# Kernel optimization log

Measured on AMD Instinct MI355X. Metric: run time of the kernel, lower is better.

The kernel has to match this reference:

```python
import jax, jax.numpy as jnp
import numpy as np

B, S, D, H = 4, 1024, 1024, 16
HD = D // H


def setup_inputs() -> dict:
    key = jax.random.key(0)
    ks = jax.random.split(key, 12)
    s = 1.0 / np.sqrt(D)
    inp = {
        'q': jax.random.normal(ks[0], (B, S, D), jnp.float32),
        'k': jax.random.normal(ks[1], (B, S, D), jnp.float32),
        'v': jax.random.normal(ks[2], (B, S, D), jnp.float32),
        'mask': jnp.broadcast_to(jnp.tril(jnp.ones((S, S), jnp.int32)), (B, S, S)),
        'Wq': jax.random.uniform(ks[3], (D, D), jnp.float32, -s, s),
        'bq': jax.random.uniform(ks[4], (D,), jnp.float32, -s, s),
        'Wk': jax.random.uniform(ks[5], (D, D), jnp.float32, -s, s),
        'bk': jax.random.uniform(ks[6], (D,), jnp.float32, -s, s),
        'Wv': jax.random.uniform(ks[7], (D, D), jnp.float32, -s, s),
        'bv': jax.random.uniform(ks[8], (D,), jnp.float32, -s, s),
        'Wo': jax.random.uniform(ks[9], (D, D), jnp.float32, -s, s),
        'bo': jax.random.uniform(ks[10], (D,), jnp.float32, -s, s),
    }
    return inp


def _split_heads(x):
    # [B,S,D] -> [B,H,S,HD]
    b, s, d = x.shape
    return x.reshape(b, s, H, HD).transpose(0, 2, 1, 3)


def reference(q, k, v, mask, Wq, bq, Wk, bk, Wv, bv, Wo, bo):
    # Linear projections (torch Linear: x @ W.T + b) followed by relu
    qh = jax.nn.relu(q @ Wq.T + bq)
    kh = jax.nn.relu(k @ Wk.T + bk)
    vh = jax.nn.relu(v @ Wv.T + bv)
    qh, kh, vh = _split_heads(qh), _split_heads(kh), _split_heads(vh)
    scores = jnp.einsum('bhqd,bhkd->bhqk', qh, kh) / jnp.sqrt(jnp.float32(HD))
    scores = jnp.where(mask[:, None, :, :] == 0, jnp.float32(-1e9), scores)
    attn = jax.nn.softmax(scores, axis=-1)
    y = jnp.einsum('bhqk,bhkd->bhqd', attn, vh)
    y = y.transpose(0, 2, 1, 3).reshape(B, S, D)  # merge heads
    return jax.nn.relu(y @ Wo.T + bo)
```

## Files before the change

### kernel.cpp

```cpp
#include <hip/hip_runtime.h>


using f16    = _Float16;
using f16x4  = __attribute__((ext_vector_type(4))) _Float16;
using f16x8  = __attribute__((ext_vector_type(8))) _Float16;
using f32x4  = __attribute__((ext_vector_type(4))) float;
using f32x16 = __attribute__((ext_vector_type(16))) float;

static constexpr int S = 1024, Dm = 1024, NH = 16, HD = 64;

#if __has_builtin(__builtin_amdgcn_mfma_f32_32x32x16_f16)
#define USE_G32 1
#define MFMA32(ACC, A_, B_) \
    (ACC) = __builtin_amdgcn_mfma_f32_32x32x16_f16((A_), (B_), (ACC), 0, 0, 0)
#else
#define USE_G32 0
#endif

#if __has_builtin(__builtin_amdgcn_mfma_f32_16x16x32_f16) && \
    __has_builtin(__builtin_amdgcn_mfma_f32_16x16x16f16)
#define USE_A16 1
#define MFMA16K32(ACC, A_, B_) \
    (ACC) = __builtin_amdgcn_mfma_f32_16x16x32_f16((A_), (B_), (ACC), 0, 0, 0)
#define MFMA16(ACC, A_, B_) \
    (ACC) = __builtin_amdgcn_mfma_f32_16x16x16f16((A_), (B_), (ACC), 0, 0, 0)
#else
#define USE_A16 0
#endif

#define LO4(v) __builtin_shufflevector((v), (v), 0, 1, 2, 3)
#define HI4(v) __builtin_shufflevector((v), (v), 4, 5, 6, 7)

__device__ __forceinline__ f16x4 cvt4(float4 a) {
    f16x4 r; r[0] = (f16)a.x; r[1] = (f16)a.y; r[2] = (f16)a.z; r[3] = (f16)a.w;
    return r;
}

__device__ __forceinline__ int pcol64(int k) {
#if USE_A16
    return ((k >> 3) & 3) * 16 + ((k >> 5) << 3) + (k & 7);
#else
    return ((k >> 2) & 3) * 16 + ((k >> 4) << 2) + (k & 3);
#endif
}

__device__ __forceinline__ int swz(int row, int col) {
    return (col & ~31) | ((((col >> 3) ^ row) & 3) << 3) | (col & 7);
}

__device__ __forceinline__ void store_out(void* out, int mode, int m, int n, float v) {
    if (mode == 2) {
        ((float*)out)[(size_t)m * Dm + n] = v;
    } else {
        const int b_ = m >> 10, s_ = m & 1023, h_ = n >> 6, hd_ = n & 63;
        const size_t idx = (mode == 0)
            ? (((size_t)(b_ * NH + h_) * S + s_) * HD + pcol64(hd_))
            : (((size_t)(b_ * NH + h_) * HD + hd_) * S + s_);
        ((f16*)out)[idx] = (f16)v;
    }
}

#if __has_builtin(__builtin_amdgcn_global_load_lds)
#define HAS_GLL 1
#else
#define HAS_GLL 0
#endif

__device__ __forceinline__ void gll16(const f16* g, f16* l) {
#if HAS_GLL
    __builtin_amdgcn_global_load_lds(
        (const __attribute__((address_space(1))) void*)g,
        (__attribute__((address_space(3))) void*)l, 16, 0, 0);
#else
    *(uint4*)l = *(const uint4*)g;
#endif
}

__global__ __launch_bounds__(256)
void cvt_w(const float* __restrict__ s0, const float* __restrict__ s1,
           const float* __restrict__ s2, f16* __restrict__ dst)
{
    const int z = blockIdx.y;
    const float* src = (z == 0) ? s0 : (z == 1) ? s1 : s2;
    const int e = blockIdx.x * 256 + threadIdx.x;
    const int n = e >> 8;
    const int k = (e & 255) * 4;
    const float4 v = *(const float4*)(src + (size_t)n * Dm + k);
    *(f16x4*)(dst + (size_t)z * Dm * Dm + (size_t)n * Dm + swz(n, k)) = cvt4(v);
}

template <int ADMA>
__device__ __forceinline__ void gemm_core(const void* __restrict__ A,
                                          const f16* __restrict__ Wf,
                                          const float* __restrict__ bias,
                                          void* __restrict__ out, int mode)
{
    const int tid = threadIdx.x;
    const int bm = blockIdx.x, bn = blockIdx.y;
#if USE_G32
    __shared__ alignas(16) f16 As[2][128][ADMA ? 32 : 36];
    __shared__ alignas(16) f16 Ws[2][128][32];

    const int lane = tid & 63, wave = tid >> 6;
    const int l31 = lane & 31, kh = lane >> 5;
    const int wm = wave & 1, wn = wave >> 1;

    const int dr = wave * 16 + (lane >> 2);
    const int dc = (lane & 3) * 8;
    const f16* Wsrc = Wf + (size_t)(bn * 128 + dr) * Dm + dc;
    const f16* Asrc = (const f16*)A + (size_t)(bm * 128 + dr) * Dm + dc;

    const int ar = tid >> 3, ac = (tid & 7) * 4;
    const float* Af = (const float*)A + (size_t)(bm * 128 + ar) * Dm + ac;

    float4 pa[4];
    auto prefA = [&](int k0) {
#pragma unroll
        for (int i = 0; i < 4; ++i) pa[i] = *(const float4*)(Af + k0 + (size_t)i * 32 * Dm);
    };
    auto stageA = [&](int cur) {
#pragma unroll
        for (int i = 0; i < 4; ++i) *(f16x4*)&As[cur][ar + i * 32][ac] = cvt4(pa[i]);
    };
    auto dma = [&](int k0, int cur) {
        gll16(Wsrc + k0, &Ws[cur][dr][dc]);
        gll16(Wsrc + k0 + (size_t)64 * Dm, &Ws[cur][64 + dr][dc]);
        if (ADMA) {
            gll16(Asrc + k0, &As[cur][dr][dc]);
            gll16(Asrc + k0 + (size_t)64 * Dm, &As[cur][64 + dr][dc]);
        }
    };

    f32x16 acc[2][2] = {};
    if (!ADMA) prefA(0);
    dma(0, 0);
    for (int it = 0; it < Dm / 32; ++it) {
        const int cur = it & 1;
        if (!ADMA) stageA(cur);
        __syncthreads();
        if (it < Dm / 32 - 1) {
            if (!ADMA) prefA((it + 1) * 32);
            dma((it + 1) * 32, cur ^ 1);
        }

#pragma unroll
        for (int s2 = 0; s2 < 2; ++s2) {
            const int sl = s2 * 2 + kh;
            f16x8 af[2], bf[2];
#pragma unroll
            for (int g = 0; g < 2; ++g) {
                const int rr = g * 32 + l31;
                const int slot = (sl ^ rr) & 3;
                if (ADMA) {
                    af[g] = *(const f16x8*)&As[cur][wm * 64 + rr][slot * 8];
                } else {
                    const int c = s2 * 16 + kh * 8;
                    const f16x4 lo = *(const f16x4*)&As[cur][wm * 64 + rr][c];
                    const f16x4 hi = *(const f16x4*)&As[cur][wm * 64 + rr][c + 4];
                    af[g] = __builtin_shufflevector(lo, hi, 0, 1, 2, 3, 4, 5, 6, 7);
                }
                bf[g] = *(const f16x8*)&Ws[cur][wn * 64 + rr][slot * 8];
            }
            MFMA32(acc[0][0], af[0], bf[0]);
            MFMA32(acc[0][1], af[0], bf[1]);
            MFMA32(acc[1][0], af[1], bf[0]);
            MFMA32(acc[1][1], af[1], bf[1]);
        }
    }

#pragma unroll
    for (int g2 = 0; g2 < 2; ++g2) {
        const int col = bn * 128 + wn * 64 + g2 * 32 + l31;
        const float bb = bias[col];
#pragma unroll
        for (int g = 0; g < 2; ++g)
#pragma unroll
            for (int blk = 0; blk < 4; ++blk) {
                const int row0 = bm * 128 + wm * 64 + g * 32 + 8 * blk + 4 * kh;
                if (mode == 1) {
                    const int b_ = row0 >> 10, s_ = row0 & 1023;
                    const int h_ = col >> 6, hd_ = col & 63;
                    f16x4 vv;
#pragma unroll
                    for (int r = 0; r < 4; ++r)
                        vv[r] = (f16)fmaxf(acc[g][g2][blk * 4 + r] + bb, 0.0f);
                    *(f16x4*)&((f16*)out)[((size_t)(b_ * NH + h_) * HD + hd_) * S + s_] = vv;
                } else {
#pragma unroll
                    for (int r = 0; r < 4; ++r)
                        store_out(out, mode, row0 + r, col,
                                  fmaxf(acc[g][g2][blk * 4 + r] + bb, 0.0f));
                }
            }
    }
#else
    for (int i = tid; i < 128 * 128; i += 256) {
        const int m = bm * 128 + (i >> 7);
        const int n = bn * 128 + (i & 127);
        float acc = 0.0f;
        for (int k2 = 0; k2 < Dm; ++k2) {
            const float a = ADMA ? (float)((const f16*)A)[(size_t)m * Dm + swz(m, k2)]
                                 : ((const float*)A)[(size_t)m * Dm + k2];
            acc = fmaf(a, (float)Wf[(size_t)n * Dm + swz(n, k2)], acc);
        }
        store_out(out, mode, m, n, fmaxf(acc + bias[n], 0.0f));
    }
#endif
}

__global__ __launch_bounds__(256)
void gemm_qkv(const float* __restrict__ q, const float* __restrict__ k,
              const float* __restrict__ v, const f16* __restrict__ wqkv,
              const float* __restrict__ bq, const float* __restrict__ bk,
              const float* __restrict__ bv,
              f16* __restrict__ qh, f16* __restrict__ kh, f16* __restrict__ vt)
{
    const int z = blockIdx.z;
    const float* A = (z == 0) ? q : (z == 1) ? k : v;
    const float* B = (z == 0) ? bq : (z == 1) ? bk : bv;
    f16* O = (z == 0) ? qh : (z == 1) ? kh : vt;
    gemm_core<0>(A, wqkv + (size_t)z * Dm * Dm, B, O, (z == 2) ? 1 : 0);
}

__global__ __launch_bounds__(256)
void gemm_out(const f16* __restrict__ y, const f16* __restrict__ wo,
              const float* __restrict__ bo, float* __restrict__ out)
{
    gemm_core<1>(y, wo, bo, out, 2);
}

__global__ __launch_bounds__(256)
void attn_fwd(const f16* __restrict__ qh, const f16* __restrict__ kh,
              const f16* __restrict__ vt, f16* __restrict__ y)
{
    const int bz = blockIdx.x;
    const int qt = bz & 15;
    const int h  = (bz >> 4) & 15;
    const int b  = bz >> 8;
    const size_t head = (size_t)(b * NH + h) * S * HD;

#if USE_A16
    __shared__ alignas(16) f16 Ks[2][64][72];
    __shared__ alignas(16) f16 Vs[2][64][72];

    const int tid  = threadIdx.x;
    const int wave = tid >> 6;
    const int lane = tid & 63;
    const int l15  = lane & 15;
    const int quad = lane >> 4;
    const int sr   = tid >> 2;
    const int sc   = (tid & 3) * 16;

    const f16* Qrow = qh + head + (size_t)(qt * 64 + wave * 16 + l15) * HD;
    const f16* Kp   = kh + head;
    const f16* Vp   = vt + head;

    f16x8 aq[2];
    {
        const uint4 q0 = *(const uint4*)(Qrow + quad * 16);
        const uint4 q1 = *(const uint4*)(Qrow + quad * 16 + 8);
        aq[0] = *(f16x8*)&q0;
        aq[1] = *(f16x8*)&q1;
    }

    const int qg = qt * 64 + wave * 16 + l15;
    float m_i = -1e30f, l_i = 0.0f;
    f32x4 acc_o[4] = {};

    uint4 pk[2], pv[2];
    auto pref = [&](int kt) {
        const f16* Kr = Kp + (size_t)(kt * 64 + sr) * HD + sc;
        pk[0] = *(const uint4*)Kr;
        pk[1] = *(const uint4*)(Kr + 8);
        const f16* Vr = Vp + (size_t)sr * S + kt * 64 + sc;
        pv[0] = *(const uint4*)Vr;
        pv[1] = *(const uint4*)(Vr + 8);
    };

    pref(0);
    for (int kt = 0; kt <= qt; ++kt) {
        const int cur = kt & 1;
        *(uint4*)&Ks[cur][sr][sc]     = pk[0];
        *(uint4*)&Ks[cur][sr][sc + 8] = pk[1];
        {
            const int sb = (sc >> 4) * 4;
            *(f16x4*)&Vs[cur][sr][0 * 16 + sb] = *(f16x4*)((f16*)&pv[0]);
            *(f16x4*)&Vs[cur][sr][1 * 16 + sb] = *(f16x4*)((f16*)&pv[0] + 4);
            *(f16x4*)&Vs[cur][sr][2 * 16 + sb] = *(f16x4*)((f16*)&pv[1]);
            *(f16x4*)&Vs[cur][sr][3 * 16 + sb] = *(f16x4*)((f16*)&pv[1] + 4);
        }
        __syncthreads();
        if (kt < qt) pref(kt + 1);

        f32x4 accs[4] = {};
#pragma unroll
        for (int t = 0; t < 4; ++t) {
            const f16x8 k8a = *(const f16x8*)&Ks[cur][t * 16 + l15][quad * 16];
            const f16x8 k8b = *(const f16x8*)&Ks[cur][t * 16 + l15][quad * 16 + 8];
            MFMA16K32(accs[t], k8a, aq[0]);
            MFMA16K32(accs[t], k8b, aq[1]);
        }

        const int key0 = kt * 64 + quad * 4;
#pragma unroll
        for (int t = 0; t < 4; ++t)
#pragma unroll
            for (int r = 0; r < 4; ++r) {
                float sv = accs[t][r] * 0.125f;
                if (key0 + t * 16 + r > qg) sv = -1e9f;
                accs[t][r] = sv;
            }

        float mx = accs[0][0];
#pragma unroll
        for (int t = 0; t < 4; ++t)
#pragma unroll
            for (int r = 0; r < 4; ++r) mx = fmaxf(mx, accs[t][r]);
        mx = fmaxf(mx, __shfl_xor(mx, 16, 64));
        mx = fmaxf(mx, __shfl_xor(mx, 32, 64));
        const float mnew = fmaxf(m_i, mx);
        float sm = 0.0f;
#pragma unroll
        for (int t = 0; t < 4; ++t)
#pragma unroll
            for (int r = 0; r < 4; ++r) {
                const float e = __expf(accs[t][r] - mnew);
                accs[t][r] = e;
                sm += e;
            }
        sm += __shfl_xor(sm, 16, 64);
        sm += __shfl_xor(sm, 32, 64);
        const float alpha = __expf(m_i - mnew);
        l_i = l_i * alpha + sm;
        m_i = mnew;

        f16x4 ap[4];
#pragma unroll
        for (int c = 0; c < 4; ++c) {
            f16x4 v;
#pragma unroll
            for (int j = 0; j < 4; ++j) v[j] = (f16)accs[c][j];
            ap[c] = v;
        }

        float ar[4];
#pragma unroll
        for (int r = 0; r < 4; ++r) ar[r] = __shfl(alpha, quad * 4 + r, 64);
#pragma unroll
        for (int t2 = 0; t2 < 4; ++t2)
#pragma unroll
            for (int r = 0; r < 4; ++r) acc_o[t2][r] *= ar[r];
#pragma unroll
        for (int t2 = 0; t2 < 4; ++t2) {
            const f16x8 v8a = *(const f16x8*)&Vs[cur][t2 * 16 + l15][quad * 16];
            const f16x8 v8b = *(const f16x8*)&Vs[cur][t2 * 16 + l15][quad * 16 + 8];
            MFMA16(acc_o[t2], ap[0], LO4(v8a));
            MFMA16(acc_o[t2], ap[1], HI4(v8a));
            MFMA16(acc_o[t2], ap[2], LO4(v8b));
            MFMA16(acc_o[t2], ap[3], HI4(v8b));
        }
    }

    float lr[4];
#pragma unroll
    for (int r = 0; r < 4; ++r) lr[r] = __shfl(l_i, quad * 4 + r, 64);
#pragma unroll
    for (int t2 = 0; t2 < 4; ++t2)
#pragma unroll
        for (int r = 0; r < 4; ++r) {
            const int srow = qt * 64 + wave * 16 + quad * 4 + r;
            const int dcol = h * 64 + t2 * 16 + l15;
            y[((size_t)b * S + srow) * Dm + swz(srow, dcol)] =
                (f16)(acc_o[t2][r] / lr[r]);
        }
#else
    const int tid = threadIdx.x;
    if (tid < 64) {
        const int q = qt * 64 + tid;
        const f16* Qr = qh + head + (size_t)q * HD;
        float qv[64];
        for (int d = 0; d < 64; ++d) qv[d] = (float)Qr[pcol64(d)];
        float mx = -1e30f;
        for (int key = 0; key <= q; ++key) {
            const f16* Kr = kh + head + (size_t)key * HD;
            float s = 0.0f;
            for (int d = 0; d < 64; ++d) s = fmaf(qv[d], (float)Kr[pcol64(d)], s);
            mx = fmaxf(mx, s * 0.125f);
        }
        float o[64];
        for (int d = 0; d < 64; ++d) o[d] = 0.0f;
        float l = 0.0f;
        for (int key = 0; key <= q; ++key) {
            const f16* Kr = kh + head + (size_t)key * HD;
            float s = 0.0f;
            for (int d = 0; d < 64; ++d) s = fmaf(qv[d], (float)Kr[pcol64(d)], s);
            const float p = __expf(s * 0.125f - mx);
            l += p;
            for (int d = 0; d < 64; ++d)
                o[d] = fmaf(p, (float)vt[head + (size_t)d * S + key], o[d]);
        }
        for (int d = 0; d < 64; ++d)
            y[((size_t)b * S + q) * Dm + swz(q, h * 64 + d)] = (f16)(o[d] / l);
    }
#endif
}

extern "C" void kernel_launch(void* const* d_in, const int* in_sizes, int n_in,
                              void* d_out, int out_size, void* d_ws, size_t ws_size,
                              hipStream_t stream)
{
    f16* ws = (f16*)d_ws;
    const size_t SEG = (size_t)4 * 1024 * 1024;
    f16* qh   = ws;
    f16* kh   = ws + SEG;
    f16* vt   = ws + 2 * SEG;
    f16* wqkv = ws + 3 * SEG;
    f16* y    = ws + 3 * SEG;
    f16* wo   = ws;

    cvt_w<<<dim3(1024, 3), 256, 0, stream>>>(
        (const float*)d_in[4], (const float*)d_in[6], (const float*)d_in[8], wqkv);
    gemm_qkv<<<dim3(32, 8, 3), 256, 0, stream>>>(
        (const float*)d_in[0], (const float*)d_in[1], (const float*)d_in[2],
        wqkv,
        (const float*)d_in[5], (const float*)d_in[7], (const float*)d_in[9],
        qh, kh, vt);
    attn_fwd<<<dim3(4 * NH * (S / 64)), 256, 0, stream>>>(qh, kh, vt, y);
    cvt_w<<<dim3(1024, 1), 256, 0, stream>>>(
        (const float*)d_in[10], nullptr, nullptr, wo);
    gemm_out<<<dim3(32, 8), 256, 0, stream>>>(
        y, wo, (const float*)d_in[11], (float*)d_out);
}
```

Measured before the change: 264.0 us.

## Double GEMM K-tile to 64 with 8-way swizzle and interleaved A staging

Raises the projection GEMM's K step from 32 to 64, halving the number of barrier iterations, and widens the LDS XOR swizzle to 8 slots to match the 64-wide rows. The fp32 A operand is now prefetched and converted in two halves interleaved between the MFMA k-slices, overlapping global loads with compute. The weight pre-conversion swizzle is changed to match. LDS use doubles, which may reduce occupancy.

```diff
diff --git a/kernel.cpp b/kernel.cpp
--- a/kernel.cpp
+++ b/kernel.cpp
@@ -45,7 +45,7 @@
 }
 
 __device__ __forceinline__ int swz(int row, int col) {
-    return (col & ~31) | ((((col >> 3) ^ row) & 3) << 3) | (col & 7);
+    return (col & ~63) | ((((col >> 3) ^ row) & 7) << 3) | (col & 7);
 }
 
 __device__ __forceinline__ void store_out(void* out, int mode, int m, int n, float v) {
@@ -98,74 +98,84 @@
     const int tid = threadIdx.x;
     const int bm = blockIdx.x, bn = blockIdx.y;
 #if USE_G32
-    __shared__ alignas(16) f16 As[2][128][ADMA ? 32 : 36];
-    __shared__ alignas(16) f16 Ws[2][128][32];
+    __shared__ alignas(16) f16 As[2][128][64];
+    __shared__ alignas(16) f16 Ws[2][128][64];
 
     const int lane = tid & 63, wave = tid >> 6;
     const int l31 = lane & 31, kh = lane >> 5;
     const int wm = wave & 1, wn = wave >> 1;
 
-    const int dr = wave * 16 + (lane >> 2);
-    const int dc = (lane & 3) * 8;
-    const f16* Wsrc = Wf + (size_t)(bn * 128 + dr) * Dm + dc;
-    const f16* Asrc = (const f16*)A + (size_t)(bm * 128 + dr) * Dm + dc;
-
-    const int ar = tid >> 3, ac = (tid & 7) * 4;
-    const float* Af = (const float*)A + (size_t)(bm * 128 + ar) * Dm + ac;
+    const int drow = lane >> 3;
+    const int dcol = (lane & 7) * 8;
+    const f16* Wsrc = Wf + (size_t)(bn * 128) * Dm + dcol;
+    const f16* Asrc = (const f16*)A + (size_t)(bm * 128) * Dm + dcol;
+
+    auto dma = [&](int k0, int cur) {
+#pragma unroll
+        for (int i = 0; i < 4; ++i) {
+            const int r = (i * 4 + wave) * 8 + drow;
+            gll16(Wsrc + (size_t)r * Dm + k0, &Ws[cur][r][dcol]);
+        }
+        if (ADMA) {
+#pragma unroll
+            for (int i = 0; i < 4; ++i) {
+                const int r = (i * 4 + wave) * 8 + drow;
+                gll16(Asrc + (size_t)r * Dm + k0, &As[cur][r][dcol]);
+            }
+        }
+    };
+
+    const int ar = tid >> 1;
+    const int ah = tid & 1;
+    const float* Af = (const float*)A + (size_t)(bm * 128 + ar) * Dm + ah * 16;
 
     float4 pa[4];
-    auto prefA = [&](int k0) {
-#pragma unroll
-        for (int i = 0; i < 4; ++i) pa[i] = *(const float4*)(Af + k0 + (size_t)i * 32 * Dm);
+    auto prefA = [&](int k0, int h) {
+#pragma unroll
+        for (int j = 0; j < 4; ++j)
+            pa[j] = *(const float4*)(Af + k0 + h * 32 + j * 4);
     };
-    auto stageA = [&](int cur) {
-#pragma unroll
-        for (int i = 0; i < 4; ++i) *(f16x4*)&As[cur][ar + i * 32][ac] = cvt4(pa[i]);
+    auto stageA = [&](int cur, int h) {
+#pragma unroll
+        for (int j2 = 0; j2 < 2; ++j2) {
+            f16x8 v;
+            const float4 a0 = pa[j2 * 2], a1 = pa[j2 * 2 + 1];
+            v[0] = (f16)a0.x; v[1] = (f16)a0.y; v[2] = (f16)a0.z; v[3] = (f16)a0.w;
+            v[4] = (f16)a1.x; v[5] = (f16)a1.y; v[6] = (f16)a1.z; v[7] = (f16)a1.w;
+            const int slot = (h * 4 + ah * 2 + j2) ^ (ar & 7);
+            *(f16x8*)&As[cur][ar][slot * 8] = v;
+        }
     };
-    auto dma = [&](int k0, int cur) {
-        gll16(Wsrc + k0, &Ws[cur][dr][dc]);
-        gll16(Wsrc + k0 + (size_t)64 * Dm, &Ws[cur][64 + dr][dc]);
-        if (ADMA) {
-            gll16(Asrc + k0, &As[cur][dr][dc]);
-            gll16(Asrc + k0 + (size_t)64 * Dm, &As[cur][64 + dr][dc]);
-        }
+
+    f32x16 acc[2][2] = {};
+
+    auto kslice = [&](int cur, int s) {
+        const int slot = ((s * 2 + kh) ^ (l31 & 7)) * 8;
+        const f16x8 af0 = *(const f16x8*)&As[cur][wm * 64 + l31][slot];
+        const f16x8 af1 = *(const f16x8*)&As[cur][wm * 64 + 32 + l31][slot];
+        const f16x8 bf0 = *(const f16x8*)&Ws[cur][wn * 64 + l31][slot];
+        const f16x8 bf1 = *(const f16x8*)&Ws[cur][wn * 64 + 32 + l31][slot];
+        MFMA32(acc[0][0], af0, bf0);
+        MFMA32(acc[0][1], af0, bf1);
+        MFMA32(acc[1][0], af1, bf0);
+        MFMA32(acc[1][1], af1, bf1);
     };
 
-    f32x16 acc[2][2] = {};
-    if (!ADMA) prefA(0);
+    constexpr int NIT = Dm / 64;
     dma(0, 0);
-    for (int it = 0; it < Dm / 32; ++it) {
+    if (!ADMA) { prefA(0, 0); stageA(0, 0); prefA(0, 1); stageA(0, 1); }
+    for (int it = 0; it < NIT; ++it) {
         const int cur = it & 1;
-        if (!ADMA) stageA(cur);
         __syncthreads();
-        if (it < Dm / 32 - 1) {
-            if (!ADMA) prefA((it + 1) * 32);
-            dma((it + 1) * 32, cur ^ 1);
-        }
-
-#pragma unroll
-        for (int s2 = 0; s2 < 2; ++s2) {
-            const int sl = s2 * 2 + kh;
-            f16x8 af[2], bf[2];
-#pragma unroll
-            for (int g = 0; g < 2; ++g) {
-                const int rr = g * 32 + l31;
-                const int slot = (sl ^ rr) & 3;
-                if (ADMA) {
-                    af[g] = *(const f16x8*)&As[cur][wm * 64 + rr][slot * 8];
-                } else {
-                    const int c = s2 * 16 + kh * 8;
-                    const f16x4 lo = *(const f16x4*)&As[cur][wm * 64 + rr][c];
-                    const f16x4 hi = *(const f16x4*)&As[cur][wm * 64 + rr][c + 4];
-                    af[g] = __builtin_shufflevector(lo, hi, 0, 1, 2, 3, 4, 5, 6, 7);
-                }
-                bf[g] = *(const f16x8*)&Ws[cur][wn * 64 + rr][slot * 8];
-            }
-            MFMA32(acc[0][0], af[0], bf[0]);
-            MFMA32(acc[0][1], af[0], bf[1]);
-            MFMA32(acc[1][0], af[1], bf[0]);
-            MFMA32(acc[1][1], af[1], bf[1]);
-        }
+        const bool more = (it < NIT - 1);
+        if (more) dma((it + 1) * 64, cur ^ 1);
+        if (!ADMA && more) prefA((it + 1) * 64, 0);
+        kslice(cur, 0);
+        kslice(cur, 1);
+        if (!ADMA && more) { stageA(cur ^ 1, 0); prefA((it + 1) * 64, 1); }
+        kslice(cur, 2);
+        if (!ADMA && more) stageA(cur ^ 1, 1);
+        kslice(cur, 3);
     }
 
 #pragma unroll
```

After: 274.6 us. 1.04x slower.
